# Kernel optimization log

Measured on AMD Instinct MI355X. Metric: run time of the kernel, lower is better.

The kernel has to match this reference:

```python
import jax, jax.numpy as jnp
import numpy as np
from jax import lax

N = 2048
P = 256
F_J = 0.05      # sparsity of recurrent matrix J
F_OUT = 0.05    # sparsity of readout
DT = 0.1
ON_TIME = 10
T = 200


def _activation(x):
    # Tanh_shifted_and_scaled: rates in [0, 1]
    return 0.5 * (1.0 + jnp.tanh(x))


def setup_inputs() -> dict:
    key = jax.random.key(0)
    k1, k2, k3, k4, k5 = jax.random.split(key, 5)
    # patterns ~ Uniform(-1, 1), shape [N, P]
    patterns = jax.random.uniform(k1, (N, P), jnp.float32, -1.0, 1.0)
    # sparse recurrent matrix J: gaussian values, density F_J, gain g
    g = 10.0 * 0.1 ** 0.25 / np.sqrt(N * P * np.sqrt(F_J))
    J_dense = jax.random.normal(k2, (N, N), jnp.float32) * jnp.float32(g)
    mask = jax.random.uniform(k3, (N, N)) < F_J
    J = jnp.where(mask, J_dense, 0.0).astype(jnp.float32)
    # sparse readout: ones at a random F_OUT fraction of units (frozen)
    w_out = (jax.random.uniform(k4, (N,)) < F_OUT).astype(jnp.float32)
    return {"patterns": patterns, "J": J, "w_out": w_out, "N_time_steps": T}


def reference(patterns, J, w_out, N_time_steps):
    # Batched over all P patterns at once (columns of [N, P] state).
    n = patterns.shape[0]
    x0 = jnp.zeros_like(patterns)           # [N, P]
    r0 = _activation(x0)

    def step(carry, ti):
        x, rates = carry
        inp = jnp.where(ti < ON_TIME, patterns, 0.0)      # [N, P]
        x = x + DT * (-x + J @ rates + inp)               # [N, P]
        rates = _activation(x)
        out_t = w_out @ rates                             # [P]
        return (x, rates), out_t

    _, outs = lax.scan(step, (x0, r0), jnp.arange(N_time_steps))  # [T, P]
    readout = outs.T / n                                   # [P, T]
    return readout
```

## Files before the change

### kernel.cpp

```cpp
#include <hip/hip_runtime.h>
#include <hip/hip_bf16.h>


#define NN 2048
#define PP 256
#define PAD 256
#define DT_C 0.1f
#define ON_TIME_C 10

__global__ void build_ell_kernel(const float* __restrict__ J,
                                 float2* __restrict__ ell,
                                 int* __restrict__ nnz) {
    int row  = blockIdx.x * (blockDim.x >> 6) + (threadIdx.x >> 6);
    int lane = threadIdx.x & 63;
    if (row >= NN) return;
    const float* Jrow = J + (size_t)row * NN;
    int base = 0;
    for (int c = 0; c < NN / 64; ++c) {
        float f = Jrow[c * 64 + lane];
        bool nz = (f != 0.0f);
        unsigned long long m = __ballot(nz);
        int pre = __popcll(m & ((1ull << lane) - 1ull));
        int pos = base + pre;
        if (nz && pos < PAD)
            ell[(size_t)row * PAD + pos] = make_float2(f, __int_as_float(c * 64 + lane));
        base += __popcll(m);
    }
    if (lane == 0) nnz[row] = (base < PAD) ? base : PAD;
}

__global__ void init_kernel(float* __restrict__ x, unsigned short* __restrict__ r,
                            float* __restrict__ out, int nout) {
    int i = blockIdx.x * blockDim.x + threadIdx.x;
    x[i] = 0.0f;
    r[i] = 0x3F00;
    if (i < nout) out[i] = 0.0f;
}

__global__ __launch_bounds__(256) void step_kernel(
    const float2* __restrict__ ell, const int* __restrict__ nnz,
    const unsigned short* __restrict__ rates_in,
    unsigned short* __restrict__ rates_out,
    float* __restrict__ x, const float* __restrict__ patterns,
    const float* __restrict__ w_out, float* __restrict__ out,
    int t, int T, int with_input) {
    int row = blockIdx.x, tid = threadIdx.x;
    int w = tid >> 6, lane = tid & 63;

    __shared__ float2 s_ell[PAD];
    __shared__ float  s_part[4][PP];

    int cnt = nnz[row];
    if (tid < cnt) s_ell[tid] = ell[(size_t)row * PAD + tid];
    __syncthreads();

    const ushort4* rin4 = (const ushort4*)rates_in;
    float4 acc = make_float4(0.f, 0.f, 0.f, 0.f);
    #pragma unroll 4
    for (int k = w; k < cnt; k += 4) {
        float2 e = s_ell[k];
        int   j  = __float_as_int(e.y);
        ushort4 rv = rin4[j * (PP / 4) + lane];
        float r0 = __uint_as_float((unsigned)rv.x << 16);
        float r1 = __uint_as_float((unsigned)rv.y << 16);
        float r2 = __uint_as_float((unsigned)rv.z << 16);
        float r3 = __uint_as_float((unsigned)rv.w << 16);
        acc.x = fmaf(e.x, r0, acc.x);
        acc.y = fmaf(e.x, r1, acc.y);
        acc.z = fmaf(e.x, r2, acc.z);
        acc.w = fmaf(e.x, r3, acc.w);
    }
    ((float4*)s_part[w])[lane] = acc;
    __syncthreads();

    float sum = s_part[0][tid] + s_part[1][tid] + s_part[2][tid] + s_part[3][tid];

    size_t off = (size_t)row * PP + tid;
    float xv  = x[off];
    float inp = with_input ? patterns[off] : 0.0f;
    xv += DT_C * (sum + inp - xv);
    x[off] = xv;
    float r = 0.5f * (1.0f + tanhf(xv));

    unsigned b  = __float_as_uint(r);
    unsigned rn = b + 0x7FFFu + ((b >> 16) & 1u);
    rates_out[off] = (unsigned short)(rn >> 16);

    if (w_out[row] != 0.0f)
        atomicAdd(&out[(size_t)tid * T + t], r * (1.0f / (float)NN));
}

extern "C" void kernel_launch(void* const* d_in, const int* in_sizes, int n_in,
                              void* d_out, int out_size, void* d_ws, size_t ws_size,
                              hipStream_t stream) {
    const float* patterns = (const float*)d_in[0];
    const float* J        = (const float*)d_in[1];
    const float* w_out    = (const float*)d_in[2];
    float* out            = (float*)d_out;

    int T = out_size / PP;

    size_t off = 0;
    auto alloc = [&](size_t bytes) {
        void* p = (char*)d_ws + off;
        off += (bytes + 255) & ~(size_t)255;
        return p;
    };
    float2*         ell = (float2*)        alloc((size_t)NN * PAD * 8);
    int*            nnz = (int*)           alloc((size_t)NN * 4);
    float*          x   = (float*)         alloc((size_t)NN * PP * 4);
    unsigned short* r0  = (unsigned short*)alloc((size_t)NN * PP * 2);
    unsigned short* r1  = (unsigned short*)alloc((size_t)NN * PP * 2);
    (void)ws_size; (void)n_in; (void)in_sizes;

    build_ell_kernel<<<NN / 4, 256, 0, stream>>>(J, ell, nnz);
    init_kernel<<<(NN * PP) / 256, 256, 0, stream>>>(x, r0, out, PP * T);

    for (int t = 0; t < T; ++t) {
        const unsigned short* rin = (t & 1) ? r1 : r0;
        unsigned short*      rout = (t & 1) ? r0 : r1;
        step_kernel<<<NN, PP, 0, stream>>>(ell, nnz, rin, rout, x, patterns,
                                           w_out, out, t, T,
                                           (t < ON_TIME_C) ? 1 : 0);
    }
}
```

Baseline: 2.114 ms.

## Pack sparse J entries as bf16 pairs and use dot2 bf16 accumulation

```diff
diff --git a/kernel.cpp b/kernel.cpp
--- a/kernel.cpp
+++ b/kernel.cpp
@@ -5,11 +5,12 @@
 #define NN 2048
 #define PP 256
 #define PAD 256
+#define NPAIR 128
 #define DT_C 0.1f
 #define ON_TIME_C 10
 
 __global__ void build_ell_kernel(const float* __restrict__ J,
-                                 float2* __restrict__ ell,
+                                 float2* __restrict__ raw,
                                  int* __restrict__ nnz) {
     int row  = blockIdx.x * (blockDim.x >> 6) + (threadIdx.x >> 6);
     int lane = threadIdx.x & 63;
@@ -23,10 +24,31 @@
         int pre = __popcll(m & ((1ull << lane) - 1ull));
         int pos = base + pre;
         if (nz && pos < PAD)
-            ell[(size_t)row * PAD + pos] = make_float2(f, __int_as_float(c * 64 + lane));
+            raw[(size_t)row * PAD + pos] = make_float2(f, __int_as_float(c * 64 + lane));
         base += __popcll(m);
     }
     if (lane == 0) nnz[row] = (base < PAD) ? base : PAD;
+}
+
+__global__ void pack_pairs_kernel(const float2* __restrict__ raw,
+                                  const int* __restrict__ nnz,
+                                  uint2* __restrict__ pairs,
+                                  int* __restrict__ npairs) {
+    int row = blockIdx.x;
+    int i   = threadIdx.x;
+    int cnt = nnz[row];
+    int npr = ((cnt + 7) / 8) * 4;
+    if (i == 0) npairs[row] = npr;
+
+    float v0 = 0.f, v1 = 0.f; int i0 = 0, i1 = 0;
+    if (2 * i < cnt)     { float2 e = raw[(size_t)row * PAD + 2 * i];     v0 = e.x; i0 = __float_as_int(e.y); }
+    if (2 * i + 1 < cnt) { float2 e = raw[(size_t)row * PAD + 2 * i + 1]; v1 = e.x; i1 = __float_as_int(e.y); }
+    unsigned b0 = __float_as_uint(v0); b0 = (b0 + 0x7FFFu + ((b0 >> 16) & 1u)) >> 16;
+    unsigned b1 = __float_as_uint(v1); b1 = (b1 + 0x7FFFu + ((b1 >> 16) & 1u)) >> 16;
+    uint2 pe;
+    pe.x = (b1 << 16) | b0;
+    pe.y = ((unsigned)i1 << 16) | (unsigned)i0;
+    pairs[(size_t)row * NPAIR + i] = pe;
 }
 
 __global__ void init_kernel(float* __restrict__ x, unsigned short* __restrict__ r,
@@ -38,7 +60,7 @@
 }
 
 __global__ __launch_bounds__(256) void step_kernel(
-    const float2* __restrict__ ell, const int* __restrict__ nnz,
+    const uint2* __restrict__ pairs, const int* __restrict__ npairs,
     const unsigned short* __restrict__ rates_in,
     unsigned short* __restrict__ rates_out,
     float* __restrict__ x, const float* __restrict__ patterns,
@@ -47,28 +69,35 @@
     int row = blockIdx.x, tid = threadIdx.x;
     int w = tid >> 6, lane = tid & 63;
 
-    __shared__ float2 s_ell[PAD];
-    __shared__ float  s_part[4][PP];
+    __shared__ uint2 s_pr[NPAIR];
+    __shared__ float s_part[4][PP];
 
-    int cnt = nnz[row];
-    if (tid < cnt) s_ell[tid] = ell[(size_t)row * PAD + tid];
+    if (tid < NPAIR) s_pr[tid] = pairs[(size_t)row * NPAIR + tid];
     __syncthreads();
 
-    const ushort4* rin4 = (const ushort4*)rates_in;
+    int npr = npairs[row];
+    int q   = npr >> 2;
+    int s0  = w * q;
+
+    const char* rbase = (const char*)rates_in + lane * 8;
     float4 acc = make_float4(0.f, 0.f, 0.f, 0.f);
-    #pragma unroll 4
-    for (int k = w; k < cnt; k += 4) {
-        float2 e = s_ell[k];
-        int   j  = __float_as_int(e.y);
-        ushort4 rv = rin4[j * (PP / 4) + lane];
-        float r0 = __uint_as_float((unsigned)rv.x << 16);
-        float r1 = __uint_as_float((unsigned)rv.y << 16);
-        float r2 = __uint_as_float((unsigned)rv.z << 16);
-        float r3 = __uint_as_float((unsigned)rv.w << 16);
-        acc.x = fmaf(e.x, r0, acc.x);
-        acc.y = fmaf(e.x, r1, acc.y);
-        acc.z = fmaf(e.x, r2, acc.z);
-        acc.w = fmaf(e.x, r3, acc.w);
+
+    #pragma unroll 2
+    for (int i = s0; i < s0 + q; ++i) {
+        uint2 e  = s_pr[i];
+        unsigned jp = e.x;
+        unsigned o0 = (e.y & 0xFFFFu) << 9;
+        unsigned o1 = (e.y >> 16) << 9;
+        uint2 q0 = *(const uint2*)(rbase + o0);
+        uint2 q1 = *(const uint2*)(rbase + o1);
+        unsigned a0 = __builtin_amdgcn_perm(q1.x, q0.x, 0x05040100u);
+        unsigned a1 = __builtin_amdgcn_perm(q1.x, q0.x, 0x07060302u);
+        unsigned a2 = __builtin_amdgcn_perm(q1.y, q0.y, 0x05040100u);
+        unsigned a3 = __builtin_amdgcn_perm(q1.y, q0.y, 0x07060302u);
+        asm("v_dot2_f32_bf16 %0, %1, %2, %0" : "+v"(acc.x) : "v"(a0), "v"(jp));
+        asm("v_dot2_f32_bf16 %0, %1, %2, %0" : "+v"(acc.y) : "v"(a1), "v"(jp));
+        asm("v_dot2_f32_bf16 %0, %1, %2, %0" : "+v"(acc.z) : "v"(a2), "v"(jp));
+        asm("v_dot2_f32_bf16 %0, %1, %2, %0" : "+v"(acc.w) : "v"(a3), "v"(jp));
     }
     ((float4*)s_part[w])[lane] = acc;
     __syncthreads();
@@ -106,20 +135,23 @@
         off += (bytes + 255) & ~(size_t)255;
         return p;
     };
-    float2*         ell = (float2*)        alloc((size_t)NN * PAD * 8);
+    float2*         raw = (float2*)        alloc((size_t)NN * PAD * 8);
     int*            nnz = (int*)           alloc((size_t)NN * 4);
+    uint2*          prs = (uint2*)         alloc((size_t)NN * NPAIR * 8);
+    int*            npr = (int*)           alloc((size_t)NN * 4);
     float*          x   = (float*)         alloc((size_t)NN * PP * 4);
     unsigned short* r0  = (unsigned short*)alloc((size_t)NN * PP * 2);
     unsigned short* r1  = (unsigned short*)alloc((size_t)NN * PP * 2);
     (void)ws_size; (void)n_in; (void)in_sizes;
 
-    build_ell_kernel<<<NN / 4, 256, 0, stream>>>(J, ell, nnz);
+    build_ell_kernel<<<NN / 4, 256, 0, stream>>>(J, raw, nnz);
+    pack_pairs_kernel<<<NN, NPAIR, 0, stream>>>(raw, nnz, prs, npr);
     init_kernel<<<(NN * PP) / 256, 256, 0, stream>>>(x, r0, out, PP * T);
 
     for (int t = 0; t < T; ++t) {
         const unsigned short* rin = (t & 1) ? r1 : r0;
         unsigned short*      rout = (t & 1) ? r0 : r1;
-        step_kernel<<<NN, PP, 0, stream>>>(ell, nnz, rin, rout, x, patterns,
+        step_kernel<<<NN, PP, 0, stream>>>(prs, npr, rin, rout, x, patterns,
                                            w_out, out, t, T,
                                            (t < ON_TIME_C) ? 1 : 0);
     }
```

After: 2.359 ms. 11.6% more time.
